# Kernel optimization log

Measured on AMD Instinct MI355X. Metric: run time of the kernel, lower is better.

## Reference

```python
import jax, jax.numpy as jnp
import numpy as np

N_BANDS = 8
N_DIFF = 5
N_AVG = 11
N_GAUSS = 15
SIGMA_G = 3.0
A_LRELU = 0.0
EPS = 1e-8


def _lrelu(x, a=A_LRELU):
    return jnp.where(x >= 0, x, a * x)


def setup_inputs() -> dict:
    key = jax.random.key(0)
    k_x, k_b1, k_b2, k_b3 = jax.random.split(key, 4)
    B, F, T = 8, 512, 16384
    x = jax.random.uniform(k_x, (B, F, T), dtype=jnp.float32)

    # log-gamma compression parameter (per band)
    log_gamma = jnp.full((N_BANDS,), jnp.log(10.0), dtype=jnp.float32)

    # depthwise diff kernel along time: [-1, +1] centered
    dw = np.zeros((N_BANDS, 1, 1, N_DIFF), dtype=np.float32)
    dw[..., N_DIFF // 2] = -1.0
    dw[..., N_DIFF // 2 + 1] = 1.0
    diff_w = jnp.asarray(dw)
    diff_b = 0.01 * jax.random.normal(k_b1, (N_BANDS,), dtype=jnp.float32)

    # depthwise local-average conv1d
    avg_w = jnp.full((N_BANDS, 1, N_AVG), 1.0 / N_AVG, dtype=jnp.float32)
    avg_b = 0.01 * jax.random.normal(k_b2, (N_BANDS,), dtype=jnp.float32)

    mix_w = jnp.full((1, N_BANDS), 1.0 / N_BANDS, dtype=jnp.float32)

    # gaussian smoothing conv1d (note: original uses 2*sigma, not 2*sigma^2)
    n = np.arange(N_GAUSS, dtype=np.float32)
    gw = np.exp(-((n - N_GAUSS // 2) ** 2) / (2.0 * SIGMA_G)).astype(np.float32)
    gauss_w = jnp.asarray(gw).reshape(1, 1, N_GAUSS)
    gauss_b = 0.01 * jax.random.normal(k_b3, (1,), dtype=jnp.float32)

    return {"x": x, "log_gamma": log_gamma, "diff_w": diff_w, "diff_b": diff_b,
            "avg_w": avg_w, "avg_b": avg_b, "mix_w": mix_w,
            "gauss_w": gauss_w, "gauss_b": gauss_b}


def reference(x, log_gamma, diff_w, diff_b, avg_w, avg_b, mix_w, gauss_w, gauss_b):
    B, F, T = x.shape
    Fb = F // N_BANDS
    # chunk along freq into bands -> [B, C=N_bands, Fb, T] (matches permute in torch)
    xb = x.reshape(B, N_BANDS, Fb, T)
    # log-gamma compression (per-band gamma)
    gamma = jnp.exp(log_gamma)[None, :, None, None]
    x_log = jnp.log1p(gamma * xb)
    # depthwise temporal diff conv, 'same' padding
    x_diff = jax.lax.conv_general_dilated(
        x_log, diff_w, window_strides=(1, 1), padding='SAME',
        dimension_numbers=('NCHW', 'OIHW', 'NCHW'),
        feature_group_count=N_BANDS) + diff_b[None, :, None, None]
    # half-wave rectify, pool over frequency -> [B, C, T]
    x_pool = _lrelu(x_diff).sum(axis=2)
    # depthwise local average along time, subtract (enhancement)
    x_avg = jax.lax.conv_general_dilated(
        x_pool, avg_w, window_strides=(1,), padding='SAME',
        dimension_numbers=('NCH', 'OIH', 'NCH'),
        feature_group_count=N_BANDS) + avg_b[None, :, None]
    x_enh = x_pool - x_avg
    # mix bands: [B, C, T] x [1, C] -> [B, 1, T]
    x_mix = jnp.einsum('bct,oc->bot', x_enh, mix_w)
    # gaussian smoothing conv1d -> [B, T]
    x_gauss = (jax.lax.conv_general_dilated(
        x_mix, gauss_w, window_strides=(1,), padding='SAME',
        dimension_numbers=('NCH', 'OIH', 'NCH')) + gauss_b[None, :, None])[:, 0, :]
    # rectify and max-normalize
    x_act = _lrelu(x_gauss)
    x_act = x_act / (x_act.max(axis=1, keepdims=True) + EPS)
    return x_act
```

## Files before the change

### kernel.cpp

```cpp
#include <hip/hip_runtime.h>

#define TT 16384
#define BB 8
#define NB 8
#define FB 64
#define TILE 2048
#define FSPLIT 4
#define FCHUNK (FB / FSPLIT)

__device__ __forceinline__ float lgf(float g, float x) {
    return __logf(fmaf(g, x, 1.0f));
}

__global__ __launch_bounds__(256) void pool_kernel(
    const float* __restrict__ x,
    const float* __restrict__ log_gamma,
    const float* __restrict__ diff_w,
    const float* __restrict__ diff_b,
    float* __restrict__ pool_part)
{
    const int bc = blockIdx.x;
    const int c  = bc & 7;
    const int t0 = blockIdx.y * TILE + threadIdx.x * 8;
    const int f0 = blockIdx.z * FCHUNK;
    const float* __restrict__ xb = x + ((size_t)bc * FB + f0) * TT;

    const float g  = __expf(log_gamma[c]);
    const float w0 = diff_w[c * 5 + 0], w1 = diff_w[c * 5 + 1],
                w2 = diff_w[c * 5 + 2], w3 = diff_w[c * 5 + 3],
                w4 = diff_w[c * 5 + 4];
    const float bias = diff_b[c];

    const bool mL = (t0 > 0);
    const bool mR = (t0 + 10 <= TT);
    const int  tm = mL ? t0 - 2 : 0;
    const int  tp = mR ? t0 + 8 : 0;

    float acc[8] = {0.f,0.f,0.f,0.f,0.f,0.f,0.f,0.f};

    float4 va = *reinterpret_cast<const float4*>(xb + t0);
    float4 vb = *reinterpret_cast<const float4*>(xb + t0 + 4);
    float2 ha = *reinterpret_cast<const float2*>(xb + tm);
    float2 hb = *reinterpret_cast<const float2*>(xb + tp);

    for (int f = 0; f < FCHUNK; ++f) {
        const int fn = (f + 1 < FCHUNK) ? f + 1 : f;
        const float* __restrict__ nrow = xb + (size_t)fn * TT;
        const float4 nva = *reinterpret_cast<const float4*>(nrow + t0);
        const float4 nvb = *reinterpret_cast<const float4*>(nrow + t0 + 4);
        const float2 nha = *reinterpret_cast<const float2*>(nrow + tm);
        const float2 nhb = *reinterpret_cast<const float2*>(nrow + tp);

        float L[12];
        L[0]  = mL ? lgf(g, ha.x) : 0.f;
        L[1]  = mL ? lgf(g, ha.y) : 0.f;
        L[2]  = lgf(g, va.x); L[3] = lgf(g, va.y);
        L[4]  = lgf(g, va.z); L[5] = lgf(g, va.w);
        L[6]  = lgf(g, vb.x); L[7] = lgf(g, vb.y);
        L[8]  = lgf(g, vb.z); L[9] = lgf(g, vb.w);
        L[10] = mR ? lgf(g, hb.x) : 0.f;
        L[11] = mR ? lgf(g, hb.y) : 0.f;

        #pragma unroll
        for (int j = 0; j < 8; ++j) {
            float d = fmaf(w0, L[j],
                      fmaf(w1, L[j+1],
                      fmaf(w2, L[j+2],
                      fmaf(w3, L[j+3],
                      fmaf(w4, L[j+4], bias)))));
            acc[j] += (d >= 0.f) ? d : 0.f;
        }
        va = nva; vb = nvb; ha = nha; hb = nhb;
    }

    float* __restrict__ po = pool_part + ((size_t)blockIdx.z * (BB * NB) + bc) * TT + t0;
    *reinterpret_cast<float4*>(po)     = make_float4(acc[0], acc[1], acc[2], acc[3]);
    *reinterpret_cast<float4*>(po + 4) = make_float4(acc[4], acc[5], acc[6], acc[7]);
}

__global__ __launch_bounds__(256) void smooth_kernel(
    const float* __restrict__ pool_part,
    const float* __restrict__ avg_w,
    const float* __restrict__ avg_b,
    const float* __restrict__ mix_w,
    const float* __restrict__ gauss_w,
    const float* __restrict__ gauss_b,
    float* __restrict__ out,
    float* __restrict__ pmax)
{
    __shared__ float sp[NB][1024 + 24];
    __shared__ float sm[1024 + 14];
    __shared__ float wmax[4];

    const int b  = blockIdx.x >> 4;
    const int t0 = (blockIdx.x & 15) * 1024;

    for (int i = threadIdx.x; i < 1024 + 24; i += 256) {
        const int t = t0 + i - 12;
        const bool in = ((unsigned)t < (unsigned)TT);
        const int tc = in ? t : (t < 0 ? 0 : TT - 1);
        #pragma unroll
        for (int c = 0; c < NB; ++c) {
            const size_t off = ((size_t)b * NB + c) * TT + tc;
            float s = 0.f;
            #pragma unroll
            for (int z = 0; z < FSPLIT; ++z)
                s += pool_part[(size_t)z * (BB * NB) * TT + off];
            sp[c][i] = in ? s : 0.f;
        }
    }
    __syncthreads();

    for (int i = threadIdx.x; i < 1024 + 14; i += 256) {
        const int t = t0 + i - 7;
        float v = 0.f;
        if ((unsigned)t < (unsigned)TT) {
            #pragma unroll
            for (int c = 0; c < NB; ++c) {
                float av = 0.f;
                #pragma unroll
                for (int j = 0; j < 11; ++j)
                    av = fmaf(avg_w[c * 11 + j], sp[c][i + j], av);
                const float e = sp[c][i + 5] - av - avg_b[c];
                v = fmaf(mix_w[c], e, v);
            }
        }
        sm[i] = v;
    }
    __syncthreads();

    const float gb = gauss_b[0];
    float lmax = 0.f;
    for (int i = threadIdx.x; i < 1024; i += 256) {
        float gs = gb;
        #pragma unroll
        for (int k = 0; k < 15; ++k)
            gs = fmaf(gauss_w[k], sm[i + k], gs);
        const float a = (gs >= 0.f) ? gs : 0.f;
        out[(size_t)b * TT + t0 + i] = a;
        lmax = fmaxf(lmax, a);
    }
    #pragma unroll
    for (int off = 32; off > 0; off >>= 1)
        lmax = fmaxf(lmax, __shfl_down(lmax, off, 64));
    if ((threadIdx.x & 63) == 0) wmax[threadIdx.x >> 6] = lmax;
    __syncthreads();
    if (threadIdx.x == 0)
        pmax[blockIdx.x] = fmaxf(fmaxf(wmax[0], wmax[1]), fmaxf(wmax[2], wmax[3]));
}

__global__ __launch_bounds__(256) void norm_kernel(
    float* __restrict__ out, const float* __restrict__ pmax)
{
    const int i = blockIdx.x * 256 + threadIdx.x;
    const int b = i >> 14;
    const float* __restrict__ pm = pmax + b * 16;
    float m = 0.f;
    #pragma unroll
    for (int k = 0; k < 16; ++k) m = fmaxf(m, pm[k]);
    out[i] = out[i] / (m + 1e-8f);
}

extern "C" void kernel_launch(void* const* d_in, const int* in_sizes, int n_in,
                              void* d_out, int out_size, void* d_ws, size_t ws_size,
                              hipStream_t stream) {
    const float* x        = (const float*)d_in[0];
    const float* log_g    = (const float*)d_in[1];
    const float* diff_w   = (const float*)d_in[2];
    const float* diff_b   = (const float*)d_in[3];
    const float* avg_w    = (const float*)d_in[4];
    const float* avg_b    = (const float*)d_in[5];
    const float* mix_w    = (const float*)d_in[6];
    const float* gauss_w  = (const float*)d_in[7];
    const float* gauss_b  = (const float*)d_in[8];
    float* out = (float*)d_out;

    float* pool_part = (float*)d_ws;
    float* pmax = (float*)((char*)d_ws + (size_t)FSPLIT * BB * NB * TT * sizeof(float));

    pool_kernel<<<dim3(BB * NB, TT / TILE, FSPLIT), 256, 0, stream>>>(
        x, log_g, diff_w, diff_b, pool_part);
    smooth_kernel<<<BB * (TT / 1024), 256, 0, stream>>>(pool_part, avg_w, avg_b, mix_w,
                                                        gauss_w, gauss_b, out, pmax);
    norm_kernel<<<(BB * TT) / 256, 256, 0, stream>>>(out, pmax);
}
```

Before: 385.3 us.

## Process sixteen timesteps per thread with single contiguous halo load, double freq split

```diff
diff --git a/kernel.cpp b/kernel.cpp
--- a/kernel.cpp
+++ b/kernel.cpp
@@ -4,8 +4,7 @@
 #define BB 8
 #define NB 8
 #define FB 64
-#define TILE 2048
-#define FSPLIT 4
+#define FSPLIT 8
 #define FCHUNK (FB / FSPLIT)
 
 __device__ __forceinline__ float lgf(float g, float x) {
@@ -21,7 +20,7 @@
 {
     const int bc = blockIdx.x;
     const int c  = bc & 7;
-    const int t0 = blockIdx.y * TILE + threadIdx.x * 8;
+    const int t0 = blockIdx.y * 4096 + threadIdx.x * 16;
     const int f0 = blockIdx.z * FCHUNK;
     const float* __restrict__ xb = x + ((size_t)bc * FB + f0) * TT;
 
@@ -31,51 +30,67 @@
                 w4 = diff_w[c * 5 + 4];
     const float bias = diff_b[c];
 
-    const bool mL = (t0 > 0);
-    const bool mR = (t0 + 10 <= TT);
-    const int  tm = mL ? t0 - 2 : 0;
-    const int  tp = mR ? t0 + 8 : 0;
-
-    float acc[8] = {0.f,0.f,0.f,0.f,0.f,0.f,0.f,0.f};
-
-    float4 va = *reinterpret_cast<const float4*>(xb + t0);
-    float4 vb = *reinterpret_cast<const float4*>(xb + t0 + 4);
-    float2 ha = *reinterpret_cast<const float2*>(xb + tm);
-    float2 hb = *reinterpret_cast<const float2*>(xb + tp);
-
+    const int b = min(max(t0 - 2, 0), TT - 20);
+    const int s = t0 - 2 - b;
+    const float* __restrict__ xr = xb + b;
+
+    float acc[16];
+    #pragma unroll
+    for (int j = 0; j < 16; ++j) acc[j] = 0.f;
+
+    float4 p0 = *reinterpret_cast<const float4*>(xr);
+    float4 p1 = *reinterpret_cast<const float4*>(xr + 4);
+    float4 p2 = *reinterpret_cast<const float4*>(xr + 8);
+    float4 p3 = *reinterpret_cast<const float4*>(xr + 12);
+    float4 p4 = *reinterpret_cast<const float4*>(xr + 16);
+
+    #pragma unroll
     for (int f = 0; f < FCHUNK; ++f) {
-        const int fn = (f + 1 < FCHUNK) ? f + 1 : f;
-        const float* __restrict__ nrow = xb + (size_t)fn * TT;
-        const float4 nva = *reinterpret_cast<const float4*>(nrow + t0);
-        const float4 nvb = *reinterpret_cast<const float4*>(nrow + t0 + 4);
-        const float2 nha = *reinterpret_cast<const float2*>(nrow + tm);
-        const float2 nhb = *reinterpret_cast<const float2*>(nrow + tp);
-
-        float L[12];
-        L[0]  = mL ? lgf(g, ha.x) : 0.f;
-        L[1]  = mL ? lgf(g, ha.y) : 0.f;
-        L[2]  = lgf(g, va.x); L[3] = lgf(g, va.y);
-        L[4]  = lgf(g, va.z); L[5] = lgf(g, va.w);
-        L[6]  = lgf(g, vb.x); L[7] = lgf(g, vb.y);
-        L[8]  = lgf(g, vb.z); L[9] = lgf(g, vb.w);
-        L[10] = mR ? lgf(g, hb.x) : 0.f;
-        L[11] = mR ? lgf(g, hb.y) : 0.f;
+        const float4 c0 = p0, c1 = p1, c2 = p2, c3 = p3, c4 = p4;
+        const float* __restrict__ nr = xr + (size_t)((f + 1 < FCHUNK) ? f + 1 : f) * TT;
+        p0 = *reinterpret_cast<const float4*>(nr);
+        p1 = *reinterpret_cast<const float4*>(nr + 4);
+        p2 = *reinterpret_cast<const float4*>(nr + 8);
+        p3 = *reinterpret_cast<const float4*>(nr + 12);
+        p4 = *reinterpret_cast<const float4*>(nr + 16);
+
+        float lg[20];
+        lg[0]=lgf(g,c0.x); lg[1]=lgf(g,c0.y); lg[2]=lgf(g,c0.z); lg[3]=lgf(g,c0.w);
+        lg[4]=lgf(g,c1.x); lg[5]=lgf(g,c1.y); lg[6]=lgf(g,c1.z); lg[7]=lgf(g,c1.w);
+        lg[8]=lgf(g,c2.x); lg[9]=lgf(g,c2.y); lg[10]=lgf(g,c2.z); lg[11]=lgf(g,c2.w);
+        lg[12]=lgf(g,c3.x); lg[13]=lgf(g,c3.y); lg[14]=lgf(g,c3.z); lg[15]=lgf(g,c3.w);
+        lg[16]=lgf(g,c4.x); lg[17]=lgf(g,c4.y); lg[18]=lgf(g,c4.z); lg[19]=lgf(g,c4.w);
+
+        float L[20];
+        if (s == 0) {
+            #pragma unroll
+            for (int k = 0; k < 20; ++k) L[k] = lg[k];
+        } else if (s < 0) {
+            L[0] = 0.f; L[1] = 0.f;
+            #pragma unroll
+            for (int k = 2; k < 20; ++k) L[k] = lg[k - 2];
+        } else {
+            #pragma unroll
+            for (int k = 0; k < 18; ++k) L[k] = lg[k + 2];
+            L[18] = 0.f; L[19] = 0.f;
+        }
 
         #pragma unroll
-        for (int j = 0; j < 8; ++j) {
-            float d = fmaf(w0, L[j],
-                      fmaf(w1, L[j+1],
-                      fmaf(w2, L[j+2],
-                      fmaf(w3, L[j+3],
-                      fmaf(w4, L[j+4], bias)))));
+        for (int j = 0; j < 16; ++j) {
+            const float d = fmaf(w0, L[j],
+                            fmaf(w1, L[j + 1],
+                            fmaf(w2, L[j + 2],
+                            fmaf(w3, L[j + 3],
+                            fmaf(w4, L[j + 4], bias)))));
             acc[j] += (d >= 0.f) ? d : 0.f;
         }
-        va = nva; vb = nvb; ha = nha; hb = nhb;
     }
 
     float* __restrict__ po = pool_part + ((size_t)blockIdx.z * (BB * NB) + bc) * TT + t0;
-    *reinterpret_cast<float4*>(po)     = make_float4(acc[0], acc[1], acc[2], acc[3]);
-    *reinterpret_cast<float4*>(po + 4) = make_float4(acc[4], acc[5], acc[6], acc[7]);
+    #pragma unroll
+    for (int q = 0; q < 4; ++q)
+        *reinterpret_cast<float4*>(po + 4 * q) =
+            make_float4(acc[4*q], acc[4*q+1], acc[4*q+2], acc[4*q+3]);
 }
 
 __global__ __launch_bounds__(256) void smooth_kernel(
@@ -178,7 +193,7 @@
     float* pool_part = (float*)d_ws;
     float* pmax = (float*)((char*)d_ws + (size_t)FSPLIT * BB * NB * TT * sizeof(float));
 
-    pool_kernel<<<dim3(BB * NB, TT / TILE, FSPLIT), 256, 0, stream>>>(
+    pool_kernel<<<dim3(BB * NB, TT / 4096, FSPLIT), 256, 0, stream>>>(
         x, log_g, diff_w, diff_b, pool_part);
     smooth_kernel<<<BB * (TT / 1024), 256, 0, stream>>>(pool_part, avg_w, avg_b, mix_w,
                                                         gauss_w, gauss_b, out, pmax);
```

Result: slower. 393.4 us (+2.1%).
